# Kernel tuning notes

Hardware: AMD Instinct MI355X
Metric: run time of the kernel (lower is better)

The kernel has to match this reference:

```python
import math
import jax, jax.numpy as jnp
import numpy as np

B, S, E, A, H, L, V = 4, 1024, 1024, 64, 16, 2, 32000
EPS = 1e-5
SCALE = math.sqrt(E)  # torch code scales by sqrt(input_dim) = sqrt(embedding_dim)
W_INIT_SCALE = 0.05   # torch.rand is U[0,1); scaled down for numerically sane softmax


def setup_inputs() -> dict:
    key = jax.random.key(0)
    ks = jax.random.split(key, 6)
    return {
        "x": jax.random.randint(ks[0], (B, S), 0, V),
        "emb": jax.random.normal(ks[1], (V, E), dtype=jnp.float32) * 0.02,
        "ln_gamma": jnp.ones((L, E), dtype=jnp.float32),
        "ln_beta": jnp.zeros((L, E), dtype=jnp.float32),
        "Wq": jax.random.uniform(ks[2], (L, H, A, E), dtype=jnp.float32) * W_INIT_SCALE,
        "Wk": jax.random.uniform(ks[3], (L, H, A, E), dtype=jnp.float32) * W_INIT_SCALE,
        "Wv": jax.random.uniform(ks[4], (L, H, E, E), dtype=jnp.float32) * W_INIT_SCALE,
    }


def _attn_layer(h, gamma, beta, wq, wk, wv):
    # h: [B,H,S,E]; LayerNorm over last dim (biased variance, like torch)
    mu = jnp.mean(h, axis=-1, keepdims=True)
    var = jnp.mean(jnp.square(h - mu), axis=-1, keepdims=True)
    hn = (h - mu) * jax.lax.rsqrt(var + EPS) * gamma + beta
    q = jnp.einsum('bhse,hae->bhsa', hn, wq)   # [B,H,S,A]
    k = jnp.einsum('bhse,hae->bhsa', hn, wk)   # [B,H,S,A]
    v = jnp.einsum('bhse,hoe->bhso', hn, wv)   # [B,H,S,E]
    scores = jnp.einsum('bhsa,bhta->bhst', q, k) / SCALE  # [B,H,S,S]
    w = jax.nn.softmax(scores, axis=-1)
    return jnp.einsum('bhst,bhto->bhso', w, v)  # [B,H,S,E]


def reference(x, emb, ln_gamma, ln_beta, Wq, Wk, Wv):
    # embed then replicate across heads: [B,S,E] -> [B,H,S,E]
    h = jnp.broadcast_to(emb[x][:, None, :, :], (B, H, S, E))
    for l in range(L):
        h = _attn_layer(h, ln_gamma[l], ln_beta[l], Wq[l], Wk[l], Wv[l])
    return h
```

## Files before the change

kernel.cpp:

```cpp
#include <hip/hip_runtime.h>

#define B_ 4
#define S_ 1024
#define E_ 1024
#define A_ 64
#define H_ 16
#define L_ 2

static constexpr float LN_EPS = 1e-5f;
static constexpr float INV_SCALE = 1.0f / 32.0f;

typedef __attribute__((ext_vector_type(8))) short bf16x8;
typedef __attribute__((ext_vector_type(4))) float f32x4;

__device__ __forceinline__ unsigned short f2bf(float f) {
  unsigned u = __float_as_uint(f);
  u += 0x7fffu + ((u >> 16) & 1u);
  return (unsigned short)(u >> 16);
}
__device__ __forceinline__ float bf2f(unsigned short s) {
  return __uint_as_float(((unsigned)s) << 16);
}

__device__ __forceinline__ float block_sum256(float v, float* red) {
#pragma unroll
  for (int o = 32; o > 0; o >>= 1) v += __shfl_down(v, o, 64);
  const int lane = threadIdx.x & 63;
  const int w = threadIdx.x >> 6;
  if (lane == 0) red[w] = v;
  __syncthreads();
  if (threadIdx.x == 0) red[0] = red[0] + red[1] + red[2] + red[3];
  __syncthreads();
  float r = red[0];
  __syncthreads();
  return r;
}

__device__ __forceinline__ float block_max256(float v, float* red) {
#pragma unroll
  for (int o = 32; o > 0; o >>= 1) v = fmaxf(v, __shfl_down(v, o, 64));
  const int lane = threadIdx.x & 63;
  const int w = threadIdx.x >> 6;
  if (lane == 0) red[w] = v;
  __syncthreads();
  if (threadIdx.x == 0) red[0] = fmaxf(fmaxf(red[0], red[1]), fmaxf(red[2], red[3]));
  __syncthreads();
  float r = red[0];
  __syncthreads();
  return r;
}

__global__ __launch_bounds__(256) void cvt_f32_bf16(const float* __restrict__ in,
                                                    unsigned short* __restrict__ out, long n) {
  long i = ((long)blockIdx.x * 256 + threadIdx.x) * 4;
  const long stride = (long)gridDim.x * 1024;
  for (; i < n; i += stride) {
    float4 v = *(const float4*)(in + i);
    ushort4 o;
    o.x = f2bf(v.x); o.y = f2bf(v.y); o.z = f2bf(v.z); o.w = f2bf(v.w);
    *(ushort4*)(out + i) = o;
  }
}

__global__ __launch_bounds__(256) void cvt_qk_concat(const float* __restrict__ Wq,
                                                     const float* __restrict__ Wk,
                                                     unsigned short* __restrict__ out) {
  const long total = (long)L_ * H_ * 128 * E_;
  long i = ((long)blockIdx.x * 256 + threadIdx.x) * 4;
  const long stride = (long)gridDim.x * 1024;
  for (; i < total; i += stride) {
    const long e = i % E_;
    const long rowhe = i / E_;
    const int row = (int)(rowhe % 128);
    const long lh = rowhe / 128;
    const float* src = (row < 64 ? Wq : Wk) + (lh * 64 + (row & 63)) * E_ + e;
    float4 v = *(const float4*)src;
    ushort4 o;
    o.x = f2bf(v.x); o.y = f2bf(v.y); o.z = f2bf(v.z); o.w = f2bf(v.w);
    *(ushort4*)(out + i) = o;
  }
}

__global__ __launch_bounds__(256) void embed_ln_kernel(
    const int* __restrict__ x, const float* __restrict__ emb,
    const float* __restrict__ gamma, const float* __restrict__ beta,
    unsigned short* __restrict__ out) {
  __shared__ float red[4];
  const int row = blockIdx.x;
  const int tid = threadIdx.x;
  const float* src = emb + (long)x[row] * E_;
  float4 v = *(const float4*)(src + tid * 4);
  const float mean = block_sum256(v.x + v.y + v.z + v.w, red) * (1.f / E_);
  float dx = v.x - mean, dy = v.y - mean, dz = v.z - mean, dw = v.w - mean;
  const float var = block_sum256(dx * dx + dy * dy + dz * dz + dw * dw, red) * (1.f / E_);
  const float rstd = rsqrtf(var + LN_EPS);
  float4 g = *(const float4*)(gamma + tid * 4);
  float4 b = *(const float4*)(beta + tid * 4);
  ushort4 o;
  o.x = f2bf(dx * rstd * g.x + b.x);
  o.y = f2bf(dy * rstd * g.y + b.y);
  o.z = f2bf(dz * rstd * g.z + b.z);
  o.w = f2bf(dw * rstd * g.w + b.w);
  *(ushort4*)(out + (long)row * E_ + tid * 4) = o;
}

__global__ __launch_bounds__(256) void ln_bf16_kernel(
    const unsigned short* __restrict__ h, const float* __restrict__ gamma,
    const float* __restrict__ beta, unsigned short* __restrict__ out) {
  __shared__ float red[4];
  const long row = blockIdx.x;
  const int tid = threadIdx.x;
  ushort4 raw = *(const ushort4*)(h + row * (long)E_ + tid * 4);
  float vx = bf2f(raw.x), vy = bf2f(raw.y), vz = bf2f(raw.z), vw = bf2f(raw.w);
  const float mean = block_sum256(vx + vy + vz + vw, red) * (1.f / E_);
  float dx = vx - mean, dy = vy - mean, dz = vz - mean, dw = vw - mean;
  const float var = block_sum256(dx * dx + dy * dy + dz * dz + dw * dw, red) * (1.f / E_);
  const float rstd = rsqrtf(var + LN_EPS);
  float4 g = *(const float4*)(gamma + tid * 4);
  float4 b = *(const float4*)(beta + tid * 4);
  ushort4 o;
  o.x = f2bf(dx * rstd * g.x + b.x);
  o.y = f2bf(dy * rstd * g.y + b.y);
  o.z = f2bf(dz * rstd * g.z + b.z);
  o.w = f2bf(dw * rstd * g.w + b.w);
  *(ushort4*)(out + row * E_ + tid * 4) = o;
}

__global__ __launch_bounds__(256) void softmax_bf16_kernel(unsigned short* __restrict__ sc) {
  __shared__ float red[4];
  unsigned short* p = sc + (long)blockIdx.x * S_;
  const int tid = threadIdx.x;
  ushort4 raw = *(const ushort4*)(p + tid * 4);
  float v0 = bf2f(raw.x), v1 = bf2f(raw.y), v2 = bf2f(raw.z), v3 = bf2f(raw.w);
  float m = block_max256(fmaxf(fmaxf(v0, v1), fmaxf(v2, v3)), red);
  v0 = __expf(v0 - m); v1 = __expf(v1 - m); v2 = __expf(v2 - m); v3 = __expf(v3 - m);
  const float s = block_sum256(v0 + v1 + v2 + v3, red);
  const float inv = 1.f / s;
  ushort4 o;
  o.x = f2bf(v0 * inv); o.y = f2bf(v1 * inv); o.z = f2bf(v2 * inv); o.w = f2bf(v3 * inv);
  *(ushort4*)(p + tid * 4) = o;
}

__device__ __forceinline__ void gload_lds16(const void* g, void* l) {
  __builtin_amdgcn_global_load_lds((const __attribute__((address_space(1))) void*)g,
                                   (__attribute__((address_space(3))) void*)l, 16, 0, 0);
}

template <int ROWS>
__device__ __forceinline__ void stage_tile(const unsigned short* __restrict__ src, int ldRow,
                                           unsigned short* lds, int tid) {
  const int rb = tid >> 3;
  const int gslot = (tid & 7) ^ (rb & 7);
  const int wbase = (tid >> 6) * 512;
#pragma unroll
  for (int i = 0; i < ROWS / 32; ++i) {
    const unsigned short* g = src + (long)(i * 32 + rb) * ldRow + gslot * 8;
    gload_lds16(g, lds + i * 2048 + wbase);
  }
}

__device__ __forceinline__ bf16x8 lds_frag(const unsigned short* base, int r, int slot) {
  const int byteoff = (r << 7) + ((slot ^ (r & 7)) << 4);
  return *(const bf16x8*)((const char*)base + byteoff);
}

template <int BM, int BN, bool OUT_BF16>
__global__ __launch_bounds__(256) void mfma_gemm_nt(
    const unsigned short* __restrict__ Aall, const unsigned short* __restrict__ Ball,
    void* __restrict__ Call, int M, int N, int K, int lda, int ldb,
    long aSB, long aSH, long bSB, long bSH, int Hn, float alpha) {
  __shared__ unsigned short As[BM * 64];
  __shared__ unsigned short Bs[BN * 64];
  const int batch = blockIdx.z;
  const int bb = batch / Hn, hh = batch % Hn;
  const unsigned short* Ap = Aall + (long)bb * aSB + (long)hh * aSH;
  const unsigned short* Bp = Ball + (long)bb * bSB + (long)hh * bSH;
  const int tid = threadIdx.x;
  const int lane = tid & 63;
  const int wave = tid >> 6;
  const int wr = wave >> 1, wc = wave & 1;
  const int bm = blockIdx.x * BM, bn = blockIdx.y * BN;
  constexpr int FM = BM / 32, FN = BN / 32;

  f32x4 acc[FM][FN];
#pragma unroll
  for (int i = 0; i < FM; ++i)
#pragma unroll
    for (int j = 0; j < FN; ++j) acc[i][j] = (f32x4)(0.f);

  for (int k0 = 0; k0 < K; k0 += 64) {
    stage_tile<BM>(Ap + (long)bm * lda + k0, lda, As, tid);
    stage_tile<BN>(Bp + (long)bn * ldb + k0, ldb, Bs, tid);
    __syncthreads();
#pragma unroll
    for (int kb = 0; kb < 2; ++kb) {
      const int slot = (kb << 2) + (lane >> 4);
      bf16x8 af[FM], bfv[FN];
#pragma unroll
      for (int mi = 0; mi < FM; ++mi)
        af[mi] = lds_frag(As, wr * (BM / 2) + mi * 16 + (lane & 15), slot);
#pragma unroll
      for (int ni = 0; ni < FN; ++ni)
        bfv[ni] = lds_frag(Bs, wc * (BN / 2) + ni * 16 + (lane & 15), slot);
#pragma unroll
      for (int mi = 0; mi < FM; ++mi)
#pragma unroll
        for (int ni = 0; ni < FN; ++ni)
          acc[mi][ni] = __builtin_amdgcn_mfma_f32_16x16x32_bf16(af[mi], bfv[ni], acc[mi][ni], 0, 0, 0);
    }
    __syncthreads();
  }

#pragma unroll
  for (int mi = 0; mi < FM; ++mi) {
    const int row = bm + wr * (BM / 2) + mi * 16 + ((lane >> 4) << 2);
#pragma unroll
    for (int ni = 0; ni < FN; ++ni) {
      const int col = bn + wc * (BN / 2) + ni * 16 + (lane & 15);
#pragma unroll
      for (int r = 0; r < 4; ++r) {
        const float v = acc[mi][ni][r] * alpha;
        const long idx = (long)batch * M * N + (long)(row + r) * N + col;
        if constexpr (OUT_BF16)
          ((unsigned short*)Call)[idx] = f2bf(v);
        else
          ((float*)Call)[idx] = v;
      }
    }
  }
}

__device__ __forceinline__ void stage_unit256(const unsigned short* __restrict__ src, int ldRow,
                                              char* lds_unit, int tid) {
#pragma unroll
  for (int i = 0; i < 2; ++i) {
    const int r = i * 128 + (tid >> 2);
    const int sg = (tid & 3) ^ ((r >> 1) & 3);
    const unsigned short* g = src + (long)r * ldRow + sg * 8;
    gload_lds16(g, lds_unit + i * 8192 + ((tid >> 6) << 10));
  }
}

__device__ __forceinline__ bf16x8 lds_frag256(const char* opbase, int kh, int r, int ss) {
  return *(const bf16x8*)(opbase + kh * 16384 + r * 64 + ((ss ^ ((r >> 1) & 3)) << 4));
}

template <bool OUT_BF16>
__global__ __launch_bounds__(512, 2) void mfma_gemm256_nt(
    const unsigned short* __restrict__ Aall, const unsigned short* __restrict__ Ball,
    void* __restrict__ Call, int M, int N, int K, int lda, int ldb,
    long aSB, long aSH, long bSB, long bSH, int Hn, float alpha) {
  extern __shared__ char lds[];
  const int nx = gridDim.x, ny = gridDim.y;
  const int nwg = nx * ny * gridDim.z;
  int f = blockIdx.x + nx * (blockIdx.y + ny * blockIdx.z);
  if ((nwg & 7) == 0) f = (f & 7) * (nwg >> 3) + (f >> 3);
  const int bx = f % nx;
  const int by = (f / nx) % ny;
  const int batch = f / (nx * ny);

  const int bb = batch / Hn, hh = batch % Hn;
  const unsigned short* Ap = Aall + (long)bb * aSB + (long)hh * aSH + (long)bx * 256 * lda;
  const unsigned short* Bp = Ball + (long)bb * bSB + (long)hh * bSH + (long)by * 256 * ldb;
  const int tid = threadIdx.x;
  const int lane = tid & 63;
  const int w = tid >> 6;
  const int wr = w >> 2, wc = w & 3;

  f32x4 acc[8][4];
#pragma unroll
  for (int i = 0; i < 8; ++i)
#pragma unroll
    for (int j = 0; j < 4; ++j) acc[i][j] = (f32x4)(0.f);

  const int NT = K >> 6;
  stage_unit256(Ap, lda, lds, tid);
  stage_unit256(Bp, ldb, lds + 32768, tid);
  stage_unit256(Ap + 32, lda, lds + 16384, tid);
  stage_unit256(Bp + 32, ldb, lds + 32768 + 16384, tid);
  asm volatile("s_waitcnt vmcnt(0)\n\ts_barrier" ::: "memory");

  for (int t = 0; t < NT; ++t) {
    const char* cur = lds + (t & 1) * 65536;
    char* nxt = lds + ((t + 1) & 1) * 65536;
    const unsigned short* An = Ap + (long)(t + 1) * 64;
    const unsigned short* Bn = Bp + (long)(t + 1) * 64;
    const bool pf = (t + 1 < NT);
#pragma unroll
    for (int kh = 0; kh < 2; ++kh) {
      bf16x8 a[8], b[4];
      const int ss = lane >> 4;
#pragma unroll
      for (int mi = 0; mi < 8; ++mi)
        a[mi] = lds_frag256(cur, kh, wr * 128 + mi * 16 + (lane & 15), ss);
#pragma unroll
      for (int ni = 0; ni < 4; ++ni)
        b[ni] = lds_frag256(cur + 32768, kh, wc * 64 + ni * 16 + (lane & 15), ss);
      if (pf) {
        stage_unit256(An + kh * 32, lda, nxt + kh * 16384, tid);
        stage_unit256(Bn + kh * 32, ldb, nxt + 32768 + kh * 16384, tid);
      }
      asm volatile("s_barrier" ::: "memory");
      __builtin_amdgcn_s_setprio(1);
#pragma unroll
      for (int mi = 0; mi < 8; ++mi)
#pragma unroll
        for (int ni = 0; ni < 4; ++ni)
          acc[mi][ni] = __builtin_amdgcn_mfma_f32_16x16x32_bf16(a[mi], b[ni], acc[mi][ni], 0, 0, 0);
      __builtin_amdgcn_s_setprio(0);
      asm volatile("s_waitcnt vmcnt(4)\n\ts_barrier" ::: "memory");
    }
  }

#pragma unroll
  for (int mi = 0; mi < 8; ++mi) {
    const int row0 = bx * 256 + wr * 128 + mi * 16 + ((lane >> 4) << 2);
#pragma unroll
    for (int ni = 0; ni < 4; ++ni) {
      const int col = by * 256 + wc * 64 + ni * 16 + (lane & 15);
#pragma unroll
      for (int r = 0; r < 4; ++r) {
        const float v = acc[mi][ni][r] * alpha;
        const long idx = (long)batch * M * N + (long)(row0 + r) * N + col;
        if constexpr (OUT_BF16)
          ((unsigned short*)Call)[idx] = f2bf(v);
        else
          ((float*)Call)[idx] = v;
      }
    }
  }
}

extern "C" void kernel_launch(void* const* d_in, const int* in_sizes, int n_in,
                              void* d_out, int out_size, void* d_ws, size_t ws_size,
                              hipStream_t stream) {
  const int* x = (const int*)d_in[0];
  const float* emb = (const float*)d_in[1];
  const float* gamma = (const float*)d_in[2];
  const float* beta = (const float*)d_in[3];
  const float* Wq = (const float*)d_in[4];
  const float* Wk = (const float*)d_in[5];
  const float* Wv = (const float*)d_in[6];
  float* out = (float*)d_out;

  (void)hipFuncSetAttribute(reinterpret_cast<const void*>(&mfma_gemm256_nt<true>),
                            hipFuncAttributeMaxDynamicSharedMemorySize, 131072);
  (void)hipFuncSetAttribute(reinterpret_cast<const void*>(&mfma_gemm256_nt<false>),
                            hipFuncAttributeMaxDynamicSharedMemorySize, 131072);

  const long WQK_N = (long)L_ * H_ * 128 * E_;
  const long WV_N = (long)L_ * H_ * E_ * E_;
  const long HN_N = (long)B_ * H_ * S_ * E_;
  const long QK_N = (long)B_ * H_ * S_ * 128;
  unsigned short* wqk = (unsigned short*)d_ws;
  unsigned short* wv_bf = wqk + WQK_N;
  unsigned short* hn = wv_bf + WV_N;
  unsigned short* qk = hn + HN_N;
  unsigned short* v_t = qk + QK_N;
  unsigned short* sc = v_t + HN_N;
  unsigned short* hid0 = (unsigned short*)d_out;

  const dim3 blk(256), blk512(512);
  const dim3 grid256(4, 4, 64);
  cvt_qk_concat<<<2048, blk, 0, stream>>>(Wq, Wk, wqk);
  cvt_f32_bf16<<<4096, blk, 0, stream>>>(Wv, wv_bf, WV_N);

  for (int l = 0; l < L_; ++l) {
    long hSB, hSH;
    if (l == 0) {
      embed_ln_kernel<<<B_ * S_, blk, 0, stream>>>(x, emb, gamma, beta, hn);
      hSB = (long)S_ * E_; hSH = 0;
    } else {
      ln_bf16_kernel<<<B_ * H_ * S_, blk, 0, stream>>>(
          hid0, gamma + (long)l * E_, beta + (long)l * E_, hn);
      hSB = (long)H_ * S_ * E_; hSH = (long)S_ * E_;
    }
    mfma_gemm_nt<128, 128, true><<<dim3(8, 1, 64), blk, 0, stream>>>(
        hn, wqk + (long)l * H_ * 128 * E_, qk, S_, 128, E_, E_, E_,
        hSB, hSH, 0L, (long)128 * E_, H_, 1.f);
    mfma_gemm256_nt<true><<<grid256, blk512, 131072, stream>>>(
        wv_bf + (long)l * H_ * E_ * E_, hn, v_t, E_, S_, E_, E_, E_,
        0L, (long)E_ * E_, hSB, hSH, H_, 1.f);
    mfma_gemm_nt<128, 128, true><<<dim3(8, 8, 64), blk, 0, stream>>>(
        qk, qk + 64, sc, S_, S_, 64, 128, 128,
        (long)H_ * S_ * 128, (long)S_ * 128, (long)H_ * S_ * 128, (long)S_ * 128, H_, INV_SCALE);
    softmax_bf16_kernel<<<B_ * H_ * S_, blk, 0, stream>>>(sc);
    if (l == 0) {
      mfma_gemm256_nt<true><<<grid256, blk512, 131072, stream>>>(
          sc, v_t, hid0, S_, E_, S_, S_, S_,
          (long)H_ * S_ * S_, (long)S_ * S_, (long)H_ * E_ * S_, (long)E_ * S_, H_, 1.f);
    } else {
      mfma_gemm256_nt<false><<<grid256, blk512, 131072, stream>>>(
          sc, v_t, out, S_, E_, S_, S_, S_,
          (long)H_ * S_ * S_, (long)S_ * S_, (long)H_ * E_ * S_, (long)E_ * S_, H_, 1.f);
    }
  }
}
```

Baseline: 1.017 ms.

## Split GEMM k-step into four finer-grained load/MFMA phases

Restructures the 256x256 bf16 GEMM main loop so each 64-wide k tile runs in four phases instead of two. Each phase loads half the A fragments and issues one global staging unit, which interleaves prefetch with MFMA more finely and reduces live fragment registers from 12 to 8 vectors. The prologue wait is also relaxed to vmcnt(4) so the loop starts before the second k-half finishes loading. Correctness depends on the vmcnt counts matching the outstanding loads per staging unit. The extra barriers add synchronization overhead.

```diff
diff --git a/kernel.cpp b/kernel.cpp
--- a/kernel.cpp
+++ b/kernel.cpp
@@ -266,6 +266,8 @@
   const int lane = tid & 63;
   const int w = tid >> 6;
   const int wr = w >> 2, wc = w & 3;
+  const int ss = lane >> 4;
+  const int ar = lane & 15;
 
   f32x4 acc[8][4];
 #pragma unroll
@@ -278,7 +280,7 @@
   stage_unit256(Bp, ldb, lds + 32768, tid);
   stage_unit256(Ap + 32, lda, lds + 16384, tid);
   stage_unit256(Bp + 32, ldb, lds + 32768 + 16384, tid);
-  asm volatile("s_waitcnt vmcnt(0)\n\ts_barrier" ::: "memory");
+  asm volatile("s_waitcnt vmcnt(4)\n\ts_barrier" ::: "memory");
 
   for (int t = 0; t < NT; ++t) {
     const char* cur = lds + (t & 1) * 65536;
@@ -286,30 +288,69 @@
     const unsigned short* An = Ap + (long)(t + 1) * 64;
     const unsigned short* Bn = Bp + (long)(t + 1) * 64;
     const bool pf = (t + 1 < NT);
-#pragma unroll
-    for (int kh = 0; kh < 2; ++kh) {
-      bf16x8 a[8], b[4];
-      const int ss = lane >> 4;
-#pragma unroll
-      for (int mi = 0; mi < 8; ++mi)
-        a[mi] = lds_frag256(cur, kh, wr * 128 + mi * 16 + (lane & 15), ss);
+    bf16x8 a[4], b[4];
+
+#pragma unroll
+    for (int ni = 0; ni < 4; ++ni)
+      b[ni] = lds_frag256(cur + 32768, 0, wc * 64 + ni * 16 + ar, ss);
+#pragma unroll
+    for (int mi = 0; mi < 4; ++mi)
+      a[mi] = lds_frag256(cur, 0, wr * 128 + mi * 16 + ar, ss);
+    if (pf) stage_unit256(An, lda, nxt, tid);
+    asm volatile("s_barrier" ::: "memory");
+    __builtin_amdgcn_s_setprio(1);
+#pragma unroll
+    for (int mi = 0; mi < 4; ++mi)
 #pragma unroll
       for (int ni = 0; ni < 4; ++ni)
-        b[ni] = lds_frag256(cur + 32768, kh, wc * 64 + ni * 16 + (lane & 15), ss);
-      if (pf) {
-        stage_unit256(An + kh * 32, lda, nxt + kh * 16384, tid);
-        stage_unit256(Bn + kh * 32, ldb, nxt + 32768 + kh * 16384, tid);
-      }
-      asm volatile("s_barrier" ::: "memory");
-      __builtin_amdgcn_s_setprio(1);
-#pragma unroll
-      for (int mi = 0; mi < 8; ++mi)
-#pragma unroll
-        for (int ni = 0; ni < 4; ++ni)
-          acc[mi][ni] = __builtin_amdgcn_mfma_f32_16x16x32_bf16(a[mi], b[ni], acc[mi][ni], 0, 0, 0);
-      __builtin_amdgcn_s_setprio(0);
-      asm volatile("s_waitcnt vmcnt(4)\n\ts_barrier" ::: "memory");
-    }
+        acc[mi][ni] = __builtin_amdgcn_mfma_f32_16x16x32_bf16(a[mi], b[ni], acc[mi][ni], 0, 0, 0);
+    __builtin_amdgcn_s_setprio(0);
+    asm volatile("s_waitcnt vmcnt(4)\n\ts_barrier" ::: "memory");
+
+#pragma unroll
+    for (int mi = 0; mi < 4; ++mi)
+      a[mi] = lds_frag256(cur, 0, wr * 128 + 64 + mi * 16 + ar, ss);
+    if (pf) stage_unit256(Bn, ldb, nxt + 32768, tid);
+    asm volatile("s_barrier" ::: "memory");
+    __builtin_amdgcn_s_setprio(1);
+#pragma unroll
+    for (int mi = 0; mi < 4; ++mi)
+#pragma unroll
+      for (int ni = 0; ni < 4; ++ni)
+        acc[4 + mi][ni] = __builtin_amdgcn_mfma_f32_16x16x32_bf16(a[mi], b[ni], acc[4 + mi][ni], 0, 0, 0);
+    __builtin_amdgcn_s_setprio(0);
+    asm volatile("s_waitcnt vmcnt(4)\n\ts_barrier" ::: "memory");
+
+#pragma unroll
+    for (int ni = 0; ni < 4; ++ni)
+      b[ni] = lds_frag256(cur + 32768, 1, wc * 64 + ni * 16 + ar, ss);
+#pragma unroll
+    for (int mi = 0; mi < 4; ++mi)
+      a[mi] = lds_frag256(cur, 1, wr * 128 + mi * 16 + ar, ss);
+    if (pf) stage_unit256(An + 32, lda, nxt + 16384, tid);
+    asm volatile("s_barrier" ::: "memory");
+    __builtin_amdgcn_s_setprio(1);
+#pragma unroll
+    for (int mi = 0; mi < 4; ++mi)
+#pragma unroll
+      for (int ni = 0; ni < 4; ++ni)
+        acc[mi][ni] = __builtin_amdgcn_mfma_f32_16x16x32_bf16(a[mi], b[ni], acc[mi][ni], 0, 0, 0);
+    __builtin_amdgcn_s_setprio(0);
+    asm volatile("s_waitcnt vmcnt(4)\n\ts_barrier" ::: "memory");
+
+#pragma unroll
+    for (int mi = 0; mi < 4; ++mi)
+      a[mi] = lds_frag256(cur, 1, wr * 128 + 64 + mi * 16 + ar, ss);
+    if (pf) stage_unit256(Bn + 32, ldb, nxt + 32768 + 16384, tid);
+    asm volatile("s_barrier" ::: "memory");
+    __builtin_amdgcn_s_setprio(1);
+#pragma unroll
+    for (int mi = 0; mi < 4; ++mi)
+#pragma unroll
+      for (int ni = 0; ni < 4; ++ni)
+        acc[4 + mi][ni] = __builtin_amdgcn_mfma_f32_16x16x32_bf16(a[mi], b[ni], acc[4 + mi][ni], 0, 0, 0);
+    __builtin_amdgcn_s_setprio(0);
+    asm volatile("s_waitcnt vmcnt(4)\n\ts_barrier" ::: "memory");
   }
 
 #pragma unroll
```

Result: faster. 975.9 us (-4.0%).
